# Optimization experiments

Measured on AMD Instinct MI355X. Metric: run time of the kernel, lower is better.

The kernel has to match this reference:

```python
import jax, jax.numpy as jnp
import numpy as np

EPS = 1e-12
BN_EPS = 1e-5

LAP = jnp.array([[0., 1., 0.], [1., -4., 1.], [0., 1., 0.]], jnp.float32).reshape(1, 1, 3, 3)
SOBX = jnp.array([[-1., 0., 1.], [-2., 0., 2.], [-1., 0., 1.]], jnp.float32).reshape(1, 1, 3, 3)
SOBY = jnp.array([[-1., -2., -1.], [0., 0., 0.], [1., 2., 1.]], jnp.float32).reshape(1, 1, 3, 3)


def _conv3x3(x, w):
    return jax.lax.conv_general_dilated(x, w, (1, 1), 'SAME',
                                        dimension_numbers=('NCHW', 'OIHW', 'NCHW'))


def _bn(x, gamma, beta, mean, var):
    # eval-mode BatchNorm2d with running stats
    inv = gamma / jnp.sqrt(var + BN_EPS)
    return x * inv[None, :, None, None] + (beta - mean * inv)[None, :, None, None]


def _entropy_u8(x01, bins=256):
    # torch.histc(min=0,max=1): bin i = [i/bins,(i+1)/bins), value==1 -> last bin
    B = x01.shape[0]
    flat = jnp.clip(x01, 0.0, 1.0).reshape(B, -1)
    idx = jnp.clip(jnp.floor(flat * bins).astype(jnp.int32), 0, bins - 1)
    h = jnp.zeros((B, bins), flat.dtype).at[jnp.arange(B)[:, None], idx].add(1.0)
    p = h / (h.sum(axis=1, keepdims=True) + EPS)
    safe_p = jnp.where(p > 0, p, 1.0)
    return jnp.where(p > 0, -p * jnp.log2(safe_p), 0.0).sum(axis=1)


def _gini(flat):
    B, N = flat.shape
    xs = jnp.sort(flat, axis=1)
    s = xs.sum(axis=1) + EPS
    w = (N + 1 - jnp.arange(1, N + 1, dtype=flat.dtype))[None, :]
    lor = (w * xs).sum(axis=1) / s
    return (N + 1 - 2.0 * lor) / N


def _grid_cv(E, grid=16):
    B, _, H, W = E.shape  # H,W divisible by grid -> adaptive_avg_pool == block mean
    pooled = E.reshape(B, grid, H // grid, grid, W // grid).mean(axis=(2, 4))
    cells = pooled.reshape(B, -1)
    return cells.std(axis=1) / (cells.mean(axis=1) + EPS)


def _lap_var(x):
    y = _conv3x3(x, LAP)
    return jnp.var(y, axis=(2, 3), ddof=1)[:, 0]  # torch .var default unbiased=True


def _sobel_mean(x):
    gx = _conv3x3(x, SOBX)
    gy = _conv3x3(x, SOBY)
    return jnp.sqrt(gx * gx + gy * gy).mean(axis=(1, 2, 3))


def _colorfulness(R, G, Bc):
    rg = (R - G)[:, 0]
    yb = ((R + G) / 2 - Bc)[:, 0]
    # torch .std default is unbiased (ddof=1)
    s = jnp.sqrt(jnp.std(rg, axis=(1, 2), ddof=1) ** 2 + jnp.std(yb, axis=(1, 2), ddof=1) ** 2)
    m = jnp.sqrt(rg.mean(axis=(1, 2)) ** 2 + yb.mean(axis=(1, 2)) ** 2)
    return s + 0.3 * m


def _metrics(img5):
    B = img5.shape[0]
    P, N = img5[:, 0:1], img5[:, 1:2]
    R, G, Bc = img5[:, 2:3], img5[:, 3:4], img5[:, 4:5]
    Pn, Nn = P / 255.0, N / 255.0
    E = jnp.maximum(Pn + Nn, 0.0)
    Y = jnp.clip(0.299 * R + 0.587 * G + 0.114 * Bc, 0.0, 1.0)
    muY = Y.mean(axis=(1, 2, 3))
    stdY = Y.std(axis=(1, 2, 3))  # unbiased=False
    flatY = Y.reshape(B, -1)
    dr = jnp.quantile(flatY, 0.99, axis=1) - jnp.quantile(flatY, 0.01, axis=1)
    psat = (Y < 0.02).astype(Y.dtype).mean(axis=(1, 2, 3)) + (Y > 0.98).astype(Y.dtype).mean(axis=(1, 2, 3))
    entY = _entropy_u8(Y)
    varlp = _lap_var(Y)
    gmean = _sobel_mean(Y)
    cf = _colorfulness(R, G, Bc)
    nz = (E > 0).astype(E.dtype).mean(axis=(1, 2, 3))
    int_density = E.mean(axis=(1, 2, 3))
    onoff = (Pn.sum(axis=(1, 2, 3)) + EPS) / (Nn.sum(axis=(1, 2, 3)) + EPS)
    gg = _gini(E.reshape(B, -1))
    cvgrid = _grid_cv(E)
    entE = _entropy_u8(E)
    varlpE = _lap_var(E)
    pbias = ((Pn - Nn) / (Pn + Nn + EPS)).mean(axis=(1, 2, 3))
    z16 = jnp.stack([muY, stdY, dr, psat, entY, varlp, gmean, cf, nz, int_density,
                     onoff, gg, cvgrid, entE, varlpE, pbias], axis=1)
    return z16[:, jnp.array([0, 1, 5, 6, 12, 9, 15, 14])]


def _forward(event, frame, conv1_w, bn1_g, bn1_b, bn1_m, bn1_v,
             conv2_w, bn2_g, bn2_b, bn2_m, bn2_v,
             fe_w1, fe_b1, fe_w2, fe_b2, hg_w, hg_b, hf_w, hf_b, res_scale):
    img5 = jnp.concatenate([event, frame], axis=1)  # (B,5,H,W)
    fx = _conv3x3(img5, conv1_w)
    fx = _bn(fx, bn1_g, bn1_b, bn1_m, bn1_v)
    fx = fx * jax.nn.sigmoid(fx)  # SiLU
    fx = _conv3x3(fx, conv2_w)
    fx = _bn(fx, bn2_g, bn2_b, bn2_m, bn2_v)
    z = jax.lax.stop_gradient(_metrics(img5))  # @torch.no_grad()
    h = jax.nn.relu(z @ fe_w1.T + fe_b1)
    h = jax.nn.relu(h @ fe_w2.T + fe_b2)
    g = jax.nn.sigmoid(h @ hg_w.T + hg_b)
    g = g / (g.sum(axis=1, keepdims=True) + EPS)
    film = h @ hf_w.T + hf_b  # (B,10)
    gamma = 1.0 + 0.1 * film[:, :5]
    beta = 0.1 * film[:, 5:]
    fx_film = gamma[:, :, None, None] * fx + beta[:, :, None, None]
    alpha = jnp.concatenate([jnp.repeat(g[:, 0:1], 2, axis=1),
                             jnp.repeat(g[:, 1:2], 3, axis=1)], axis=1)
    fused = fx_film * alpha[:, :, None, None]
    out5 = img5 + res_scale[0] * fused
    return out5


def setup_inputs() -> dict:
    key = jax.random.key(0)
    ks = jax.random.split(key, 21)
    B, H, W = 16, 512, 512
    CH, HID, MD = 16, 64, 8
    u = lambda k, s, off=0.0: jax.random.uniform(k, s, jnp.float32) + off
    n = lambda k, s, sc=0.1: jax.random.normal(k, s, jnp.float32) * sc
    return {
        'event': u(ks[0], (B, 2, H, W)),
        'frame': u(ks[1], (B, 3, H, W)),
        'conv1_w': n(ks[2], (CH, 5, 3, 3)),
        'bn1_g': u(ks[3], (CH,), 0.5), 'bn1_b': n(ks[4], (CH,)),
        'bn1_m': n(ks[5], (CH,)), 'bn1_v': u(ks[6], (CH,), 0.5),
        'conv2_w': n(ks[7], (5, CH, 3, 3)),
        'bn2_g': u(ks[8], (5,), 0.5), 'bn2_b': n(ks[9], (5,)),
        'bn2_m': n(ks[10], (5,)), 'bn2_v': u(ks[11], (5,), 0.5),
        'fe_w1': n(ks[12], (HID, MD)), 'fe_b1': n(ks[13], (HID,)),
        'fe_w2': n(ks[14], (HID, HID)), 'fe_b2': n(ks[15], (HID,)),
        'hg_w': n(ks[16], (2, HID)), 'hg_b': n(ks[17], (2,)),
        'hf_w': n(ks[18], (10, HID)), 'hf_b': n(ks[19], (10,)),
        'res_scale': n(ks[20], (1,)),
    }


def reference(event, frame, conv1_w, bn1_g, bn1_b, bn1_m, bn1_v,
              conv2_w, bn2_g, bn2_b, bn2_m, bn2_v,
              fe_w1, fe_b1, fe_w2, fe_b2, hg_w, hg_b, hf_w, hf_b, res_scale):
    out5 = _forward(event, frame, conv1_w, bn1_g, bn1_b, bn1_m, bn1_v,
                    conv2_w, bn2_g, bn2_b, bn2_m, bn2_v,
                    fe_w1, fe_b1, fe_w2, fe_b2, hg_w, hg_b, hf_w, hf_b, res_scale)
    return out5[:, 0:2], out5[:, 2:5]
```

## Files before the change

### kernel.cpp

```cpp
#include <hip/hip_runtime.h>
#include <hip/hip_bf16.h>

typedef unsigned int   u32;
typedef unsigned short u16;

#define HW 262144
#define W512 512

typedef __attribute__((ext_vector_type(8))) short short8;
typedef __attribute__((ext_vector_type(4))) float f32x4;

__device__ __forceinline__ u32 f2b_rtne(float f) {
    union { float f; u32 i; } c; c.f = f;
    u32 u = c.i;
    return (u + 0x7FFFu + ((u >> 16) & 1u)) >> 16;
}
__device__ __forceinline__ u32 pk_bf16(float lo, float hi) {
    float2 t; t.x = lo; t.y = hi;
    __hip_bfloat162 h = __float22bfloat162_rn(t);
    return *reinterpret_cast<u32*>(&h);
}
__device__ __forceinline__ float lo16(u32 w) {
    union { u32 i; float f; } c; c.i = w << 16; return c.f;
}
__device__ __forceinline__ float hi16(u32 w) {
    union { u32 i; float f; } c; c.i = w & 0xFFFF0000u; return c.f;
}
__device__ __forceinline__ float silu_fast(float v) {
    return v * __builtin_amdgcn_rcpf(1.f + __expf(-v));
}

__device__ __forceinline__ void row6(const u16* rowp, int base, float* o) {
    uint2 A = *reinterpret_cast<const uint2*>(rowp + base - 4);
    uint2 B = *reinterpret_cast<const uint2*>(rowp + base);
    uint2 C = *reinterpret_cast<const uint2*>(rowp + base + 4);
    o[0] = hi16(A.y);
    o[1] = lo16(B.x); o[2] = hi16(B.x);
    o[3] = lo16(B.y); o[4] = hi16(B.y);
    o[5] = lo16(C.x);
}

__global__ __launch_bounds__(1024) void k_band(
    const float* __restrict__ ev, const float* __restrict__ fr,
    int nb, float* __restrict__ partials, float* __restrict__ z)
{
    __shared__ u16 sYb[18][528];
    __shared__ u16 sEb[18][528];
    __shared__ float cellPart[1024];
    __shared__ float cellFull[256];
    __shared__ float red[16][8];

    int blk = blockIdx.x;
    int b = blk / nb, band = blk % nb;
    int rowsPerBand = 512 / nb;
    int chunks = rowsPerBand >> 4;
    int rBase = band * rowsPerBand;
    int tid = threadIdx.x;

    const float* Pp = ev + (size_t)(b * 2)     * HW;
    const float* Np = ev + (size_t)(b * 2 + 1) * HW;
    const float* Rp = fr + (size_t)(b * 3)     * HW;
    const float* Gp = fr + (size_t)(b * 3 + 1) * HW;
    const float* Bp = fr + (size_t)(b * 3 + 2) * HW;

    if (nb == 1 && tid < 256) cellFull[tid] = 0.f;
    if (tid < 36) {
        int rr = tid >> 1, side = tid & 1;
        uint4 zz = {0, 0, 0, 0};
        *reinterpret_cast<uint4*>(&sYb[rr][side ? 520 : 0]) = zz;
        *reinterpret_cast<uint4*>(&sEb[rr][side ? 520 : 0]) = zz;
    }

    float aY = 0, aY2 = 0, aL = 0, aL2 = 0, aG = 0, aPb = 0, aLE = 0, aLE2 = 0;

    for (int ch = 0; ch < chunks; ++ch) {
        int r0 = rBase + ch * 16;
        __syncthreads();
        for (int idx = tid; idx < 2304; idx += 1024) {
            int rl = idx >> 7, q4 = (idx & 127) << 2;
            int gy = r0 - 1 + rl;
            float4 y4 = {0.f, 0.f, 0.f, 0.f};
            float4 e4 = {0.f, 0.f, 0.f, 0.f};
            if (gy >= 0 && gy < W512) {
                size_t o = (size_t)gy * W512 + q4;
                float4 R = *reinterpret_cast<const float4*>(Rp + o);
                float4 G = *reinterpret_cast<const float4*>(Gp + o);
                float4 B = *reinterpret_cast<const float4*>(Bp + o);
                float4 P = *reinterpret_cast<const float4*>(Pp + o);
                float4 N = *reinterpret_cast<const float4*>(Np + o);
                y4.x = fminf(fmaxf(0.299f * R.x + 0.587f * G.x + 0.114f * B.x, 0.f), 1.f);
                y4.y = fminf(fmaxf(0.299f * R.y + 0.587f * G.y + 0.114f * B.y, 0.f), 1.f);
                y4.z = fminf(fmaxf(0.299f * R.z + 0.587f * G.z + 0.114f * B.z, 0.f), 1.f);
                y4.w = fminf(fmaxf(0.299f * R.w + 0.587f * G.w + 0.114f * B.w, 0.f), 1.f);
                e4.x = fmaxf((P.x + N.x) * (1.f / 255.f), 0.f);
                e4.y = fmaxf((P.y + N.y) * (1.f / 255.f), 0.f);
                e4.z = fmaxf((P.z + N.z) * (1.f / 255.f), 0.f);
                e4.w = fmaxf((P.w + N.w) * (1.f / 255.f), 0.f);
                if (rl >= 1 && rl <= 16) {
                    float pnx = P.x * (1.f / 255.f), nnx = N.x * (1.f / 255.f);
                    float pny = P.y * (1.f / 255.f), nny = N.y * (1.f / 255.f);
                    float pnz = P.z * (1.f / 255.f), nnz = N.z * (1.f / 255.f);
                    float pnw = P.w * (1.f / 255.f), nnw = N.w * (1.f / 255.f);
                    aPb += (pnx - nnx) * __builtin_amdgcn_rcpf(pnx + nnx + 1e-12f);
                    aPb += (pny - nny) * __builtin_amdgcn_rcpf(pny + nny + 1e-12f);
                    aPb += (pnz - nnz) * __builtin_amdgcn_rcpf(pnz + nnz + 1e-12f);
                    aPb += (pnw - nnw) * __builtin_amdgcn_rcpf(pnw + nnw + 1e-12f);
                }
            }
            uint2 py, pe;
            py.x = pk_bf16(y4.x, y4.y); py.y = pk_bf16(y4.z, y4.w);
            pe.x = pk_bf16(e4.x, e4.y); pe.y = pk_bf16(e4.z, e4.w);
            *reinterpret_cast<uint2*>(&sYb[rl][8 + q4]) = py;
            *reinterpret_cast<uint2*>(&sEb[rl][8 + q4]) = pe;
        }
        __syncthreads();

        float ce = 0.f;
        #pragma unroll
        for (int q = 0; q < 2; ++q) {
            int qi = tid + (q << 10);
            int row = qi >> 7, c4 = (qi & 127) << 2;
            int lr = row + 1, base = 8 + c4;
            float y0[6], y1[6], y2[6], er[6];
            row6(&sYb[lr - 1][0], base, y0);
            row6(&sYb[lr][0],     base, y1);
            row6(&sYb[lr + 1][0], base, y2);
            row6(&sEb[lr][0],     base, er);
            uint2 U = *reinterpret_cast<const uint2*>(&sEb[lr - 1][base]);
            uint2 D = *reinterpret_cast<const uint2*>(&sEb[lr + 1][base]);
            float eu[4] = {lo16(U.x), hi16(U.x), lo16(U.y), hi16(U.y)};
            float ed[4] = {lo16(D.x), hi16(D.x), lo16(D.y), hi16(D.y)};
            #pragma unroll
            for (int j = 0; j < 4; ++j) {
                float y = y1[j + 1];
                float lap = y0[j + 1] + y2[j + 1] + y1[j] + y1[j + 2] - 4.f * y;
                float gx  = (y0[j + 2] + 2.f * y1[j + 2] + y2[j + 2])
                          - (y0[j]     + 2.f * y1[j]     + y2[j]);
                float gy2 = (y2[j] + 2.f * y2[j + 1] + y2[j + 2])
                          - (y0[j] + 2.f * y0[j + 1] + y0[j + 2]);
                float gm = sqrtf(gx * gx + gy2 * gy2);
                float e = er[j + 1];
                float lapE = eu[j] + ed[j] + er[j] + er[j + 2] - 4.f * e;
                aY += y; aY2 += y * y; aL += lap; aL2 += lap * lap; aG += gm;
                aLE += lapE; aLE2 += lapE * lapE; ce += e;
            }
        }
        cellPart[tid] = ce;
        __syncthreads();
        if (tid < 16) {
            float s = 0.f;
            for (int rg = 0; rg < 8; ++rg)
                for (int k = 0; k < 8; ++k)
                    s += cellPart[rg * 128 + tid * 8 + k];
            if (nb == 1) cellFull[(r0 >> 5) * 16 + tid] += s;
            else         partials[(size_t)blk * 32 + 9 + tid] = s;
        }
    }
    __syncthreads();

    float v[8] = {aY, aY2, aL, aL2, aG, aPb, aLE, aLE2};
    #pragma unroll
    for (int off = 32; off; off >>= 1)
        #pragma unroll
        for (int k = 0; k < 8; ++k) v[k] += __shfl_down(v[k], off);
    int lane = tid & 63, wid = tid >> 6;
    if (lane == 0)
        for (int k = 0; k < 8; ++k) red[wid][k] = v[k];
    __syncthreads();

    if (tid == 0) {
        float s[8];
        for (int k = 0; k < 8; ++k) {
            float t = 0.f;
            for (int w = 0; w < 16; ++w) t += red[w][k];
            s[k] = t;
        }
        if (nb > 1) {
            float* rec = partials + (size_t)blk * 32;
            for (int k = 0; k < 8; ++k) rec[k] = s[k];
        } else {
            float c1 = 0.f, c2 = 0.f, ct = 0.f;
            for (int j = 0; j < 256; ++j) {
                float m = cellFull[j] * (1.f / 1024.f);
                c1 += m; c2 += m * m; ct += cellFull[j];
            }
            const float FN = 262144.f;
            float muY   = s[0] / FN;
            float stdY  = sqrtf(fmaxf(s[1] / FN - muY * muY, 0.f));
            float varlp = fmaxf(s[3] - s[2] * s[2] / FN, 0.f) / (FN - 1.f);
            float gmean = s[4] / FN;
            float mc = c1 * (1.f / 256.f);
            float vc = fmaxf(c2 * (1.f / 256.f) - mc * mc, 0.f);
            float cv = sqrtf(vc) / (mc + 1e-12f);
            float dens = ct / FN;
            float pb = s[5] / FN;
            float varlpE = fmaxf(s[7] - s[6] * s[6] / FN, 0.f) / (FN - 1.f);
            float* zb = z + b * 8;
            zb[0] = muY; zb[1] = stdY; zb[2] = varlp; zb[3] = gmean;
            zb[4] = cv;  zb[5] = dens; zb[6] = pb;    zb[7] = varlpE;
        }
    }
}

__global__ __launch_bounds__(256) void k_finalize(
    const float* __restrict__ partials, float* __restrict__ z)
{
    __shared__ float sred[8];
    __shared__ float rr[4][3];
    int b = blockIdx.x, tid = threadIdx.x;
    if (tid < 8) {
        float s = 0.f;
        for (int band = 0; band < 32; ++band)
            s += partials[(size_t)(b * 32 + band) * 32 + tid];
        sred[tid] = s;
    }
    int cr = tid >> 4, cc = tid & 15;
    float cell = partials[(size_t)(b * 32 + 2 * cr)     * 32 + 9 + cc]
               + partials[(size_t)(b * 32 + 2 * cr + 1) * 32 + 9 + cc];
    float m = cell * (1.f / 1024.f);
    float c1 = m, c2 = m * m, ct = cell;
    #pragma unroll
    for (int off = 32; off; off >>= 1) {
        c1 += __shfl_down(c1, off);
        c2 += __shfl_down(c2, off);
        ct += __shfl_down(ct, off);
    }
    int lane = tid & 63, wid = tid >> 6;
    if (lane == 0) { rr[wid][0] = c1; rr[wid][1] = c2; rr[wid][2] = ct; }
    __syncthreads();
    if (tid == 0) {
        float C1 = rr[0][0] + rr[1][0] + rr[2][0] + rr[3][0];
        float C2 = rr[0][1] + rr[1][1] + rr[2][1] + rr[3][1];
        float CT = rr[0][2] + rr[1][2] + rr[2][2] + rr[3][2];
        const float FN = 262144.f;
        float muY   = sred[0] / FN;
        float stdY  = sqrtf(fmaxf(sred[1] / FN - muY * muY, 0.f));
        float varlp = fmaxf(sred[3] - sred[2] * sred[2] / FN, 0.f) / (FN - 1.f);
        float gmean = sred[4] / FN;
        float mc = C1 * (1.f / 256.f);
        float vc = fmaxf(C2 * (1.f / 256.f) - mc * mc, 0.f);
        float cv = sqrtf(vc) / (mc + 1e-12f);
        float dens = CT / FN;
        float pb = sred[5] / FN;
        float varlpE = fmaxf(sred[7] - sred[6] * sred[6] / FN, 0.f) / (FN - 1.f);
        float* zb = z + b * 8;
        zb[0] = muY; zb[1] = stdY; zb[2] = varlp; zb[3] = gmean;
        zb[4] = cv;  zb[5] = dens; zb[6] = pb;    zb[7] = varlpE;
    }
}

__global__ __launch_bounds__(1024) void k_mlp(
    const float* __restrict__ z,
    const float* __restrict__ w1, const float* __restrict__ b1,
    const float* __restrict__ w2, const float* __restrict__ b2,
    const float* __restrict__ hgw, const float* __restrict__ hgb,
    const float* __restrict__ hfw, const float* __restrict__ hfb,
    const float* __restrict__ rs,
    const float* __restrict__ c1w,
    const float* __restrict__ bn1g, const float* __restrict__ bn1b,
    const float* __restrict__ bn1m, const float* __restrict__ bn1v,
    const float* __restrict__ c2w,
    const float* __restrict__ bn2g, const float* __restrict__ bn2b,
    const float* __restrict__ bn2m, const float* __restrict__ bn2v,
    float* __restrict__ coefA, float* __restrict__ cBp,
    u16* __restrict__ w1frag, u16* __restrict__ w2frag,
    float* __restrict__ b1f)
{
    int j = threadIdx.x, b = threadIdx.y;
    int ft = b * 64 + j;

    for (int t = ft; t < 1536; t += 1024) {
        int m = t >> 9, ln = (t >> 3) & 63, sl = t & 7;
        int oc = ln & 15, gg = ln >> 4;
        int tap = m * 4 + gg;
        float v = 0.f;
        if (tap < 9 && sl < 5)
            v = c1w[oc * 45 + sl * 9 + tap] * (bn1g[oc] * rsqrtf(bn1v[oc] + 1e-5f));
        w1frag[t] = (u16)f2b_rtne(v);
    }
    for (int t = ft; t < 2560; t += 1024) {
        int m = t >> 9, ln = (t >> 3) & 63, sl = t & 7;
        int oc = ln & 15, gg = ln >> 4;
        int tap = 2 * m + (gg >> 1);
        int ic = (gg & 1) * 8 + sl;
        float v = 0.f;
        if (oc < 5 && tap < 9)
            v = c2w[oc * 144 + ic * 9 + tap] * (bn2g[oc] * rsqrtf(bn2v[oc] + 1e-5f));
        w2frag[t] = (u16)f2b_rtne(v);
    }
    if (ft < 16) {
        float inv = bn1g[ft] * rsqrtf(bn1v[ft] + 1e-5f);
        b1f[ft] = bn1b[ft] - bn1m[ft] * inv;
    }

    __shared__ float sZ[16][8], sH1[16][64], sH2[16][64], sG[16][2], sF[16][10];
    if (j < 8) sZ[b][j] = z[b * 8 + j];
    __syncthreads();
    float a = b1[j];
    #pragma unroll
    for (int k = 0; k < 8; ++k) a += sZ[b][k] * w1[j * 8 + k];
    sH1[b][j] = fmaxf(a, 0.f);
    __syncthreads();
    float a2 = b2[j];
    for (int k = 0; k < 64; ++k) a2 += sH1[b][k] * w2[j * 64 + k];
    sH2[b][j] = fmaxf(a2, 0.f);
    __syncthreads();
    if (j < 2) {
        float g = hgb[j];
        for (int k = 0; k < 64; ++k) g += sH2[b][k] * hgw[j * 64 + k];
        sG[b][j] = 1.f / (1.f + __expf(-g));
    }
    if (j < 10) {
        float f = hfb[j];
        for (int k = 0; k < 64; ++k) f += sH2[b][k] * hfw[j * 64 + k];
        sF[b][j] = f;
    }
    __syncthreads();
    if (j < 5) {
        float gs = sG[b][0] + sG[b][1] + 1e-12f;
        float alpha = (j < 2 ? sG[b][0] : sG[b][1]) / gs;
        float gamma = 1.f + 0.1f * sF[b][j];
        float beta  = 0.1f * sF[b][5 + j];
        float r = rs[0];
        float inv2 = bn2g[j] * rsqrtf(bn2v[j] + 1e-5f);
        float b2fold = bn2b[j] - bn2m[j] * inv2;
        float cA = r * alpha * gamma;
        coefA[b * 5 + j] = cA;
        cBp[b * 5 + j]   = r * alpha * beta + cA * b2fold;
    }
}

__global__ __launch_bounds__(256, 3) void k_main(
    const float* __restrict__ ev, const float* __restrict__ fr,
    const u16* __restrict__ w1frag, const u16* __restrict__ w2frag,
    const float* __restrict__ b1f,
    const float* __restrict__ coefA, const float* __restrict__ cBp,
    float* __restrict__ out)
{
    __shared__ __align__(16) u16 sIn[20 * 40 * 8];
    __shared__ __align__(16) u16 sT1[18 * 34 * 24];

    int tid = threadIdx.x;
    int lane = tid & 63, wv = tid >> 6;
    int g = lane >> 4, col = lane & 15;
    int b = blockIdx.z;
    int ty0 = blockIdx.y * 16, tx0 = blockIdx.x * 32;

    const float* p0 = ev + (size_t)(b * 2)     * HW;
    const float* p1 = ev + (size_t)(b * 2 + 1) * HW;
    const float* p2 = fr + (size_t)(b * 3)     * HW;
    const float* p3 = fr + (size_t)(b * 3 + 1) * HW;
    const float* p4 = fr + (size_t)(b * 3 + 2) * HW;

    if (tid < 200) {
        int r = tid / 10, k = tid % 10;
        int gy = ty0 - 2 + r, gx = tx0 - 4 + 4 * k;
        float4 v0 = {0,0,0,0}, v1 = {0,0,0,0}, v2 = {0,0,0,0}, v3 = {0,0,0,0}, v4 = {0,0,0,0};
        if (gy >= 0 && gy < W512 && gx >= 0 && gx < W512) {
            size_t o = (size_t)gy * W512 + gx;
            v0 = *reinterpret_cast<const float4*>(p0 + o);
            v1 = *reinterpret_cast<const float4*>(p1 + o);
            v2 = *reinterpret_cast<const float4*>(p2 + o);
            v3 = *reinterpret_cast<const float4*>(p3 + o);
            v4 = *reinterpret_cast<const float4*>(p4 + o);
        }
        int base = (r * 40 + 4 * k) * 8;
        const float* a0 = (const float*)&v0;
        const float* a1 = (const float*)&v1;
        const float* a2 = (const float*)&v2;
        const float* a3 = (const float*)&v3;
        const float* a4 = (const float*)&v4;
        #pragma unroll
        for (int jx = 0; jx < 4; ++jx) {
            uint4 pk;
            pk.x = pk_bf16(a0[jx], a1[jx]);
            pk.y = pk_bf16(a2[jx], a3[jx]);
            pk.z = pk_bf16(a4[jx], 0.f);
            pk.w = 0;
            *reinterpret_cast<uint4*>(&sIn[base + jx * 8]) = pk;
        }
    }

    short8 a1f[3], a2f[5];
    #pragma unroll
    for (int m = 0; m < 3; ++m)
        a1f[m] = *reinterpret_cast<const short8*>(&w1frag[(m * 64 + lane) * 8]);
    #pragma unroll
    for (int m = 0; m < 5; ++m)
        a2f[m] = *reinterpret_cast<const short8*>(&w2frag[(m * 64 + lane) * 8]);
    f32x4 b1v = *reinterpret_cast<const f32x4*>(&b1f[g * 4]);

    int boff1[3];
    #pragma unroll
    for (int m = 0; m < 3; ++m) {
        int tap = m * 4 + g; if (tap > 8) tap = 8;
        boff1[m] = ((tap / 3) * 40 + (tap % 3)) * 16;
    }
    int boff2[5];
    #pragma unroll
    for (int m = 0; m < 5; ++m) {
        int tap = 2 * m + (g >> 1); if (tap > 8) tap = 8;
        boff2[m] = ((tap / 3) * 34 + (tap % 3)) * 48 + (g & 1) * 16;
    }

    __syncthreads();

    for (int t = wv; t < 39; t += 8) {
        bool hasB = (t + 4 < 39);
        int qA = t * 16 + col;
        int qB = hasB ? (qA + 64) : qA;
        int qcA = qA > 611 ? 611 : qA;
        int qcB = qB > 611 ? 611 : qB;
        int rA = qcA / 34, cA = qcA - rA * 34;
        int rB = qcB / 34, cB = qcB - rB * 34;
        const char* baseA = (const char*)&sIn[(rA * 40 + cA + 2) * 8];
        const char* baseB = (const char*)&sIn[(rB * 40 + cB + 2) * 8];
        short8 fA0 = *reinterpret_cast<const short8*>(baseA + boff1[0]);
        short8 fB0 = *reinterpret_cast<const short8*>(baseB + boff1[0]);
        short8 fA1 = *reinterpret_cast<const short8*>(baseA + boff1[1]);
        short8 fB1 = *reinterpret_cast<const short8*>(baseB + boff1[1]);
        short8 fA2 = *reinterpret_cast<const short8*>(baseA + boff1[2]);
        short8 fB2 = *reinterpret_cast<const short8*>(baseB + boff1[2]);
        f32x4 accA = {0.f, 0.f, 0.f, 0.f};
        f32x4 accB = {0.f, 0.f, 0.f, 0.f};
        accA = __builtin_amdgcn_mfma_f32_16x16x32_bf16(a1f[0], fA0, accA, 0, 0, 0);
        accB = __builtin_amdgcn_mfma_f32_16x16x32_bf16(a1f[0], fB0, accB, 0, 0, 0);
        accA = __builtin_amdgcn_mfma_f32_16x16x32_bf16(a1f[1], fA1, accA, 0, 0, 0);
        accB = __builtin_amdgcn_mfma_f32_16x16x32_bf16(a1f[1], fB1, accB, 0, 0, 0);
        accA = __builtin_amdgcn_mfma_f32_16x16x32_bf16(a1f[2], fA2, accA, 0, 0, 0);
        accB = __builtin_amdgcn_mfma_f32_16x16x32_bf16(a1f[2], fB2, accB, 0, 0, 0);

        {
            int gy1 = ty0 - 1 + rA, gx1 = tx0 - 1 + cA;
            bool inimg = (gy1 >= 0 && gy1 < W512 && gx1 >= 0 && gx1 < W512);
            float v0 = silu_fast(accA[0] + b1v[0]);
            float v1 = silu_fast(accA[1] + b1v[1]);
            float v2 = silu_fast(accA[2] + b1v[2]);
            float v3 = silu_fast(accA[3] + b1v[3]);
            if (!inimg) { v0 = v1 = v2 = v3 = 0.f; }
            uint2 pk;
            pk.x = pk_bf16(v0, v1);
            pk.y = pk_bf16(v2, v3);
            *reinterpret_cast<uint2*>(&sT1[(rA * 34 + cA) * 24 + g * 4]) = pk;
        }
        if (hasB) {
            int gy1 = ty0 - 1 + rB, gx1 = tx0 - 1 + cB;
            bool inimg = (gy1 >= 0 && gy1 < W512 && gx1 >= 0 && gx1 < W512);
            float v0 = silu_fast(accB[0] + b1v[0]);
            float v1 = silu_fast(accB[1] + b1v[1]);
            float v2 = silu_fast(accB[2] + b1v[2]);
            float v3 = silu_fast(accB[3] + b1v[3]);
            if (!inimg) { v0 = v1 = v2 = v3 = 0.f; }
            uint2 pk;
            pk.x = pk_bf16(v0, v1);
            pk.y = pk_bf16(v2, v3);
            *reinterpret_cast<uint2*>(&sT1[(rB * 34 + cB) * 24 + g * 4]) = pk;
        }
    }
    __syncthreads();

    float cA0 = coefA[b * 5 + 0], cA1 = coefA[b * 5 + 1], cA2 = coefA[b * 5 + 2];
    float cA3 = coefA[b * 5 + 3], cA4 = coefA[b * 5 + 4];
    float cB0 = cBp[b * 5 + 0], cB1 = cBp[b * 5 + 1], cB2 = cBp[b * 5 + 2];
    float cB3 = cBp[b * 5 + 3], cB4 = cBp[b * 5 + 4];
    const size_t OUT2 = (size_t)32 * HW;

    for (int t = wv; t < 32; t += 8) {
        int qA = t * 16 + col;
        int qB = qA + 64;
        int rA = qA >> 5, cA = qA & 31;
        int rB = qB >> 5, cB = qB & 31;
        const char* baseA = (const char*)&sT1[(rA * 34 + cA) * 24];
        const char* baseB = (const char*)&sT1[(rB * 34 + cB) * 24];
        f32x4 accA = {0.f, 0.f, 0.f, 0.f};
        f32x4 accB = {0.f, 0.f, 0.f, 0.f};
        #pragma unroll
        for (int m = 0; m < 5; ++m) {
            short8 fA = *reinterpret_cast<const short8*>(baseA + boff2[m]);
            short8 fB = *reinterpret_cast<const short8*>(baseB + boff2[m]);
            accA = __builtin_amdgcn_mfma_f32_16x16x32_bf16(a2f[m], fA, accA, 0, 0, 0);
            accB = __builtin_amdgcn_mfma_f32_16x16x32_bf16(a2f[m], fB, accB, 0, 0, 0);
        }
        size_t pxA = (size_t)(ty0 + rA) * W512 + (tx0 + cA);
        size_t pxB = (size_t)(ty0 + rB) * W512 + (tx0 + cB);
        if (g == 0) {
            out[(size_t)(b * 2 + 0) * HW + pxA] = p0[pxA] + cA0 * accA[0] + cB0;
            out[(size_t)(b * 2 + 0) * HW + pxB] = p0[pxB] + cA0 * accB[0] + cB0;
            out[(size_t)(b * 2 + 1) * HW + pxA] = p1[pxA] + cA1 * accA[1] + cB1;
            out[(size_t)(b * 2 + 1) * HW + pxB] = p1[pxB] + cA1 * accB[1] + cB1;
            out[OUT2 + (size_t)(b * 3 + 0) * HW + pxA] = p2[pxA] + cA2 * accA[2] + cB2;
            out[OUT2 + (size_t)(b * 3 + 0) * HW + pxB] = p2[pxB] + cA2 * accB[2] + cB2;
            out[OUT2 + (size_t)(b * 3 + 1) * HW + pxA] = p3[pxA] + cA3 * accA[3] + cB3;
            out[OUT2 + (size_t)(b * 3 + 1) * HW + pxB] = p3[pxB] + cA3 * accB[3] + cB3;
        } else if (g == 1) {
            out[OUT2 + (size_t)(b * 3 + 2) * HW + pxA] = p4[pxA] + cA4 * accA[0] + cB4;
            out[OUT2 + (size_t)(b * 3 + 2) * HW + pxB] = p4[pxB] + cA4 * accB[0] + cB4;
        }
    }
}

extern "C" void kernel_launch(void* const* d_in, const int* in_sizes, int n_in,
                              void* d_out, int out_size, void* d_ws, size_t ws_size,
                              hipStream_t stream)
{
    const float* ev = (const float*)d_in[0];
    const float* fr = (const float*)d_in[1];

    char* wb = (char*)d_ws;
    float* coefA    = (float*)(wb + 0);
    float* cBp      = (float*)(wb + 320);
    float* b1f      = (float*)(wb + 640);
    u16*   w1frag   = (u16*) (wb + 768);
    u16*   w2frag   = (u16*) (wb + 3840);
    float* zbuf     = (float*)(wb + 8960);
    float* partials = (float*)(wb + 10240);

    bool fast = (ws_size >= 75776);
    int nb   = fast ? 32 : 1;
    int nblk = fast ? 512 : 16;
    k_band<<<dim3(nblk), dim3(1024), 0, stream>>>(ev, fr, nb, partials, zbuf);
    if (fast) k_finalize<<<dim3(16), dim3(256), 0, stream>>>(partials, zbuf);

    k_mlp<<<dim3(1), dim3(64, 16), 0, stream>>>(zbuf,
        (const float*)d_in[12], (const float*)d_in[13], (const float*)d_in[14], (const float*)d_in[15],
        (const float*)d_in[16], (const float*)d_in[17], (const float*)d_in[18], (const float*)d_in[19],
        (const float*)d_in[20],
        (const float*)d_in[2], (const float*)d_in[3], (const float*)d_in[4], (const float*)d_in[5],
        (const float*)d_in[6], (const float*)d_in[7], (const float*)d_in[8], (const float*)d_in[9],
        (const float*)d_in[10], (const float*)d_in[11],
        coefA, cBp, w1frag, w2frag, b1f);

    k_main<<<dim3(16, 32, 16), dim3(256), 0, stream>>>(ev, fr,
        w1frag, w2frag, b1f, coefA, cBp, (float*)d_out);
}
```

Measured before the change: 140.7 us.

## Shrink sT1 stride, fold bias into MFMA init, fast-path interior tiles, raise occupancy

```diff
diff --git a/kernel.cpp b/kernel.cpp
--- a/kernel.cpp
+++ b/kernel.cpp
@@ -330,7 +330,7 @@
     }
 }
 
-__global__ __launch_bounds__(256, 3) void k_main(
+__global__ __launch_bounds__(256, 4) void k_main(
     const float* __restrict__ ev, const float* __restrict__ fr,
     const u16* __restrict__ w1frag, const u16* __restrict__ w2frag,
     const float* __restrict__ b1f,
@@ -338,13 +338,15 @@
     float* __restrict__ out)
 {
     __shared__ __align__(16) u16 sIn[20 * 40 * 8];
-    __shared__ __align__(16) u16 sT1[18 * 34 * 24];
+    __shared__ __align__(16) u16 sT1[18 * 34 * 16];
 
     int tid = threadIdx.x;
     int lane = tid & 63, wv = tid >> 6;
     int g = lane >> 4, col = lane & 15;
     int b = blockIdx.z;
     int ty0 = blockIdx.y * 16, tx0 = blockIdx.x * 32;
+    bool interior = (blockIdx.x >= 1 && blockIdx.x <= 14 &&
+                     blockIdx.y >= 1 && blockIdx.y <= 30);
 
     const float* p0 = ev + (size_t)(b * 2)     * HW;
     const float* p1 = ev + (size_t)(b * 2 + 1) * HW;
@@ -355,14 +357,24 @@
     if (tid < 200) {
         int r = tid / 10, k = tid % 10;
         int gy = ty0 - 2 + r, gx = tx0 - 4 + 4 * k;
-        float4 v0 = {0,0,0,0}, v1 = {0,0,0,0}, v2 = {0,0,0,0}, v3 = {0,0,0,0}, v4 = {0,0,0,0};
-        if (gy >= 0 && gy < W512 && gx >= 0 && gx < W512) {
+        float4 v0, v1, v2, v3, v4;
+        if (interior) {
             size_t o = (size_t)gy * W512 + gx;
             v0 = *reinterpret_cast<const float4*>(p0 + o);
             v1 = *reinterpret_cast<const float4*>(p1 + o);
             v2 = *reinterpret_cast<const float4*>(p2 + o);
             v3 = *reinterpret_cast<const float4*>(p3 + o);
             v4 = *reinterpret_cast<const float4*>(p4 + o);
+        } else {
+            v0 = v1 = v2 = v3 = v4 = float4{0, 0, 0, 0};
+            if (gy >= 0 && gy < W512 && gx >= 0 && gx < W512) {
+                size_t o = (size_t)gy * W512 + gx;
+                v0 = *reinterpret_cast<const float4*>(p0 + o);
+                v1 = *reinterpret_cast<const float4*>(p1 + o);
+                v2 = *reinterpret_cast<const float4*>(p2 + o);
+                v3 = *reinterpret_cast<const float4*>(p3 + o);
+                v4 = *reinterpret_cast<const float4*>(p4 + o);
+            }
         }
         int base = (r * 40 + 4 * k) * 8;
         const float* a0 = (const float*)&v0;
@@ -400,7 +412,7 @@
     #pragma unroll
     for (int m = 0; m < 5; ++m) {
         int tap = 2 * m + (g >> 1); if (tap > 8) tap = 8;
-        boff2[m] = ((tap / 3) * 34 + (tap % 3)) * 48 + (g & 1) * 16;
+        boff2[m] = ((tap / 3) * 34 + (tap % 3)) * 32 + (g & 1) * 16;
     }
 
     __syncthreads();
@@ -421,8 +433,8 @@
         short8 fB1 = *reinterpret_cast<const short8*>(baseB + boff1[1]);
         short8 fA2 = *reinterpret_cast<const short8*>(baseA + boff1[2]);
         short8 fB2 = *reinterpret_cast<const short8*>(baseB + boff1[2]);
-        f32x4 accA = {0.f, 0.f, 0.f, 0.f};
-        f32x4 accB = {0.f, 0.f, 0.f, 0.f};
+        f32x4 accA = b1v;
+        f32x4 accB = b1v;
         accA = __builtin_amdgcn_mfma_f32_16x16x32_bf16(a1f[0], fA0, accA, 0, 0, 0);
         accB = __builtin_amdgcn_mfma_f32_16x16x32_bf16(a1f[0], fB0, accB, 0, 0, 0);
         accA = __builtin_amdgcn_mfma_f32_16x16x32_bf16(a1f[1], fA1, accA, 0, 0, 0);
@@ -431,30 +443,34 @@
         accB = __builtin_amdgcn_mfma_f32_16x16x32_bf16(a1f[2], fB2, accB, 0, 0, 0);
 
         {
-            int gy1 = ty0 - 1 + rA, gx1 = tx0 - 1 + cA;
-            bool inimg = (gy1 >= 0 && gy1 < W512 && gx1 >= 0 && gx1 < W512);
-            float v0 = silu_fast(accA[0] + b1v[0]);
-            float v1 = silu_fast(accA[1] + b1v[1]);
-            float v2 = silu_fast(accA[2] + b1v[2]);
-            float v3 = silu_fast(accA[3] + b1v[3]);
-            if (!inimg) { v0 = v1 = v2 = v3 = 0.f; }
+            float v0 = silu_fast(accA[0]);
+            float v1 = silu_fast(accA[1]);
+            float v2 = silu_fast(accA[2]);
+            float v3 = silu_fast(accA[3]);
+            if (!interior) {
+                int gy1 = ty0 - 1 + rA, gx1 = tx0 - 1 + cA;
+                bool inimg = (gy1 >= 0 && gy1 < W512 && gx1 >= 0 && gx1 < W512);
+                if (!inimg) { v0 = v1 = v2 = v3 = 0.f; }
+            }
             uint2 pk;
             pk.x = pk_bf16(v0, v1);
             pk.y = pk_bf16(v2, v3);
-            *reinterpret_cast<uint2*>(&sT1[(rA * 34 + cA) * 24 + g * 4]) = pk;
+            *reinterpret_cast<uint2*>(&sT1[(rA * 34 + cA) * 16 + g * 4]) = pk;
         }
         if (hasB) {
-            int gy1 = ty0 - 1 + rB, gx1 = tx0 - 1 + cB;
-            bool inimg = (gy1 >= 0 && gy1 < W512 && gx1 >= 0 && gx1 < W512);
-            float v0 = silu_fast(accB[0] + b1v[0]);
-            float v1 = silu_fast(accB[1] + b1v[1]);
-            float v2 = silu_fast(accB[2] + b1v[2]);
-            float v3 = silu_fast(accB[3] + b1v[3]);
-            if (!inimg) { v0 = v1 = v2 = v3 = 0.f; }
+            float v0 = silu_fast(accB[0]);
+            float v1 = silu_fast(accB[1]);
+            float v2 = silu_fast(accB[2]);
+            float v3 = silu_fast(accB[3]);
+            if (!interior) {
+                int gy1 = ty0 - 1 + rB, gx1 = tx0 - 1 + cB;
+                bool inimg = (gy1 >= 0 && gy1 < W512 && gx1 >= 0 && gx1 < W512);
+                if (!inimg) { v0 = v1 = v2 = v3 = 0.f; }
+            }
             uint2 pk;
             pk.x = pk_bf16(v0, v1);
             pk.y = pk_bf16(v2, v3);
-            *reinterpret_cast<uint2*>(&sT1[(rB * 34 + cB) * 24 + g * 4]) = pk;
+            *reinterpret_cast<uint2*>(&sT1[(rB * 34 + cB) * 16 + g * 4]) = pk;
         }
     }
     __syncthreads();
@@ -470,8 +486,8 @@
         int qB = qA + 64;
         int rA = qA >> 5, cA = qA & 31;
         int rB = qB >> 5, cB = qB & 31;
-        const char* baseA = (const char*)&sT1[(rA * 34 + cA) * 24];
-        const char* baseB = (const char*)&sT1[(rB * 34 + cB) * 24];
+        const char* baseA = (const char*)&sT1[(rA * 34 + cA) * 16];
+        const char* baseB = (const char*)&sT1[(rB * 34 + cB) * 16];
         f32x4 accA = {0.f, 0.f, 0.f, 0.f};
         f32x4 accB = {0.f, 0.f, 0.f, 0.f};
         #pragma unroll
```

Result: faster. 128.8 us (-8.5%).
